# Optimization experiments

Hardware: AMD Instinct MI355X
Metric: run time of the kernel (lower is better)

Reference implementation:

```python
import jax, jax.numpy as jnp
import numpy as np

B, T, C, HD = 4, 4096, 2048, 128  # batch, block_size, n_embadding, head_dim


def _precompute_cos_sin(dim, end, theta=10000.0):
    freqs = 1.0 / theta ** (np.arange(0, dim, 2)[: dim // 2].astype(np.float32) / dim)
    t = np.arange(end, dtype=np.float32)
    ang = np.outer(t, freqs)  # [T, HD/2]
    return jnp.asarray(np.cos(ang), jnp.float32), jnp.asarray(np.sin(ang), jnp.float32)


def setup_inputs() -> dict:
    key = jax.random.key(0)
    k0, k1, k2, k3 = jax.random.split(key, 4)
    scale = 1.0 / np.sqrt(C).astype(np.float32)
    x = jax.random.normal(k0, (B, T, C), jnp.float32)
    Wq = jax.random.normal(k1, (HD, C), jnp.float32) * scale
    Wk = jax.random.normal(k2, (HD, C), jnp.float32) * scale
    Wv = jax.random.normal(k3, (HD, C), jnp.float32) * scale
    cos, sin = _precompute_cos_sin(HD, T)
    return {"x": x, "Wq": Wq, "Wk": Wk, "Wv": Wv, "cos": cos, "sin": sin}


def _rope(v, cos, sin):
    # v: [B, T, HD]; complex multiply on (even, odd) pairs
    v2 = v.reshape(*v.shape[:-1], -1, 2)  # [B, T, HD/2, 2]
    vr, vi = v2[..., 0], v2[..., 1]
    c = cos[None, :, :]  # [1, T, HD/2]
    s = sin[None, :, :]
    out_r = vr * c - vi * s
    out_i = vr * s + vi * c
    return jnp.stack([out_r, out_i], axis=-1).reshape(v.shape)


def reference(x, Wq, Wk, Wv, cos, sin):
    Bx, Tx, Cx = x.shape
    q = jnp.einsum('btc,dc->btd', x, Wq)
    k = jnp.einsum('btc,dc->btd', x, Wk)
    q = _rope(q, cos, sin)
    k = _rope(k, cos, sin)
    # NOTE: original scales by full embedding dim C, not head_dim
    scores = jnp.einsum('btd,bsd->bts', q, k) * (Cx ** -0.5)
    causal = jnp.tril(jnp.ones((Tx, Tx), bool))
    scores = jnp.where(causal[None, :, :], scores, -jnp.inf)
    w = jax.nn.softmax(scores, axis=-1)
    v = jnp.einsum('btc,dc->btd', x, Wv)
    return jnp.einsum('bts,bsd->btd', w, v)
```

## Files before the change

kernel.cpp:

```cpp
#include <hip/hip_runtime.h>

#define B_ 4
#define T_ 4096
#define C_ 2048
#define HD_ 128
#define M_ (B_*T_)

typedef __bf16 bf8 __attribute__((ext_vector_type(8)));
typedef __bf16 bf16x2 __attribute__((ext_vector_type(2)));
typedef __bf16 bf16x4 __attribute__((ext_vector_type(4)));
typedef unsigned short u16x8 __attribute__((ext_vector_type(8)));
typedef unsigned short u16x4 __attribute__((ext_vector_type(4)));
typedef float f32x4 __attribute__((ext_vector_type(4)));

typedef __attribute__((address_space(3))) unsigned char lds_u8_t;
typedef __attribute__((address_space(1))) const unsigned char gm_u8_t;

__device__ __forceinline__ void glds16(const void* g, void* l) {
    __builtin_amdgcn_global_load_lds((gm_u8_t*)g, (lds_u8_t*)l, 16, 0, 0);
}

__device__ __forceinline__ bf8 cvt_bf8(float4 a, float4 b) {
    bf8 t;
    t[0]=(__bf16)a.x; t[1]=(__bf16)a.y; t[2]=(__bf16)a.z; t[3]=(__bf16)a.w;
    t[4]=(__bf16)b.x; t[5]=(__bf16)b.y; t[6]=(__bf16)b.z; t[7]=(__bf16)b.w;
    return t;
}
__device__ __forceinline__ unsigned pk2(float a, float b) {
    bf16x2 t; t[0] = (__bf16)a; t[1] = (__bf16)b;
    return __builtin_bit_cast(unsigned, t);
}
__device__ __forceinline__ u16x4 pk4(float a, float b, float c, float d) {
    bf16x4 t; t[0]=(__bf16)a; t[1]=(__bf16)b; t[2]=(__bf16)c; t[3]=(__bf16)d;
    return __builtin_bit_cast(u16x4, t);
}
__device__ __forceinline__ bf8 ld_bf8(const unsigned short* p) {
    u16x8 t = *(const u16x8*)p;
    return __builtin_bit_cast(bf8, t);
}
__device__ __forceinline__ float bf2f(unsigned short h) {
    unsigned u = ((unsigned)h) << 16;
    return __builtin_bit_cast(float, u);
}
__device__ __forceinline__ f32x4 zero4() { f32x4 v = {0.f,0.f,0.f,0.f}; return v; }

__global__ __launch_bounds__(256) void wconv(
    const float* __restrict__ Wq, const float* __restrict__ Wk,
    const float* __restrict__ Wv, unsigned short* __restrict__ wbf)
{
    int idx = blockIdx.x * 256 + threadIdx.x;
    int e = idx * 8;
    int z = e >> 18;
    int r = e & 262143;
    const float* src = (z == 0 ? Wq : z == 1 ? Wk : Wv) + r;
    float4 a = *(const float4*)src;
    float4 b = *(const float4*)(src + 4);
    bf8 o = cvt_bf8(a, b);
    *(u16x8*)(wbf + e) = __builtin_bit_cast(u16x8, o);
}

__global__ __launch_bounds__(256) void qkv_gemm(
    const float* __restrict__ x, const unsigned short* __restrict__ wbf,
    const float* __restrict__ cosp, const float* __restrict__ sinp,
    unsigned short* __restrict__ qws, unsigned short* __restrict__ kws,
    unsigned short* __restrict__ vws)
{
    __shared__ __align__(16) float xs[2][64*64];
    __shared__ __align__(16) unsigned short ws2[2][128*64];

    const int tid = threadIdx.x;
    const int w = tid >> 6, l = tid & 63;
    const int g = blockIdx.x;
    const int xcd = g & 7;
    const int s = g >> 3;
    const int z = s % 3;
    const int mm = s / 3;
    const int mt = mm * 8 + xcd;
    const int rowbase = mt * 64;

    const int swz = l & 7;
    const int aq  = l >> 4;
    const int coll = l & 15;

    f32x4 acc[2][4];
    #pragma unroll
    for (int i = 0; i < 2; ++i)
        #pragma unroll
        for (int j = 0; j < 4; ++j) acc[i][j] = zero4();

    const unsigned short* wsrc = wbf + (size_t)z * (HD_ * C_);

    auto stage = [&](int buf, int kc) {
        #pragma unroll
        for (int c = 0; c < 4; ++c) {
            int row = w * 16 + c * 4 + aq;
            int fb = coll ^ (row & 7);
            glds16(x + (size_t)(rowbase + row) * C_ + kc + fb * 4,
                   (void*)&xs[buf][(w * 16 + c * 4) * 64]);
        }
        #pragma unroll
        for (int c = 0; c < 4; ++c) {
            int row = w * 32 + c * 8 + (l >> 3);
            int fb = (l & 7) ^ (row & 7);
            glds16(wsrc + (size_t)row * C_ + kc + fb * 8,
                   (void*)&ws2[buf][(w * 32 + c * 8) * 64]);
        }
    };

    stage(0, 0);

    for (int it = 0; it < 32; ++it) {
        __syncthreads();
        if (it + 1 < 32) stage((it + 1) & 1, (it + 1) * 64);
        const float* xcur = xs[it & 1];
        const unsigned short* wcur = ws2[it & 1];

        #pragma unroll
        for (int ks_ = 0; ks_ < 2; ++ks_) {
            bf8 a[2];
            #pragma unroll
            for (int mi = 0; mi < 2; ++mi) {
                int row = (w & 1) * 32 + mi * 16 + coll;
                int s0 = ks_ * 8 + aq * 2;
                float4 fa = *(const float4*)&xcur[row * 64 + ((s0 ^ swz) << 2)];
                float4 fb = *(const float4*)&xcur[row * 64 + (((s0 + 1) ^ swz) << 2)];
                a[mi] = cvt_bf8(fa, fb);
            }
            #pragma unroll
            for (int nt = 0; nt < 4; ++nt) {
                int row = (w >> 1) * 64 + nt * 16 + coll;
                int slot = (ks_ * 4 + aq) ^ swz;
                bf8 bb = ld_bf8(&wcur[row * 64 + (slot << 3)]);
                acc[0][nt] = __builtin_amdgcn_mfma_f32_16x16x32_bf16(a[0], bb, acc[0][nt], 0, 0, 0);
                acc[1][nt] = __builtin_amdgcn_mfma_f32_16x16x32_bf16(a[1], bb, acc[1][nt], 0, 0, 0);
            }
        }
    }

    const int rl0 = aq * 4;
    const int cbase = (w >> 1) * 64;
    const int mrow = (w & 1) * 32;
    if (z < 2) {
        const float QSC = 0.022097086912079608f * 1.44269504088896340736f;
        const float fs = (z == 0) ? QSC : 1.0f;
        unsigned short* dst = (z == 0) ? qws : kws;
        #pragma unroll
        for (int mi = 0; mi < 2; ++mi) {
            #pragma unroll
            for (int nt = 0; nt < 4; ++nt) {
                int col = cbase + nt * 16 + coll;
                #pragma unroll
                for (int r = 0; r < 4; ++r) {
                    float val = acc[mi][nt][r];
                    float oth = __shfl_xor(val, 1, 64);
                    int grow = rowbase + mrow + mi * 16 + rl0 + r;
                    int t = grow & (T_ - 1);
                    if ((coll & 1) == 0) {
                        int i = col >> 1;
                        float cv = cosp[t * 64 + i], sv = sinp[t * 64 + i];
                        float o_r = (val * cv - oth * sv) * fs;
                        float o_i = (val * sv + oth * cv) * fs;
                        *(unsigned*)&dst[(size_t)grow * HD_ + col] = pk2(o_r, o_i);
                    }
                }
            }
        }
    } else {
        const int bq = rowbase >> 12;
        #pragma unroll
        for (int mi = 0; mi < 2; ++mi) {
            int tb = (rowbase + mrow + mi * 16 + rl0) & (T_ - 1);
            #pragma unroll
            for (int nt = 0; nt < 4; ++nt) {
                int col = cbase + nt * 16 + coll;
                u16x4 pk = pk4(acc[mi][nt][0], acc[mi][nt][1], acc[mi][nt][2], acc[mi][nt][3]);
                *(u16x4*)&vws[(size_t)(bq * HD_ + col) * T_ + tb] = pk;
            }
        }
    }
}

__global__ __launch_bounds__(256) void attn_part(
    const unsigned short* __restrict__ qws, const unsigned short* __restrict__ kws,
    const unsigned short* __restrict__ vws,
    unsigned short* __restrict__ partO, float* __restrict__ partL)
{
    __shared__ __align__(16) unsigned short ks[2][64*128];
    __shared__ __align__(16) unsigned short vs[2][128*64];
    __shared__ __align__(16) unsigned short ps[4*16*72];

    const int tid = threadIdx.x;
    const int w = tid >> 6, l = tid & 63;
    const int id = blockIdx.x;
    const int xcd = id & 7;
    const int b = xcd >> 1;
    const int j = (id >> 3) * 2 + (xcd & 1);
    const int sp = 287 - j;
    int g = 0;
    while (4 * (g + 1) * (g + 2) <= sp) ++g;
    const int r_ = sp - 4 * g * (g + 1);
    const int qdiv = r_ / (g + 1);
    const int qt = 8 * g + qdiv;
    const int c  = r_ - qdiv * (g + 1);
    const int ntiles = (c < g) ? 8 : ((qt & 7) + 1);
    const int slot = b * 288 + 4 * g * (g + 1) + (qt & 7) * (g + 1) + c;
    const int qbase = qt * 64;
    const int cbase = c * 512;
    const size_t rowoff = (size_t)b * T_;

    const int swz = l & 7, aq = l >> 4, coll = l & 15;
    unsigned short* psw = ps + w * (16 * 72);

    bf8 qf[4];
    {
        const unsigned short* qp = qws + (rowoff + qbase + w * 16 + coll) * HD_ + aq * 8;
        #pragma unroll
        for (int kk = 0; kk < 4; ++kk) qf[kk] = ld_bf8(qp + kk * 32);
    }

    auto stageKV = [&](int buf, int st) {
        const int sbase = cbase + st * 64;
        #pragma unroll
        for (int cc = 0; cc < 4; ++cc) {
            int row = w * 16 + cc * 4 + aq;
            int fb = coll ^ (row & 7);
            glds16(kws + (rowoff + sbase + row) * HD_ + fb * 8,
                   (void*)&ks[buf][(w * 16 + cc * 4) * 128]);
        }
        #pragma unroll
        for (int cc = 0; cc < 4; ++cc) {
            int row = w * 32 + cc * 8 + (l >> 3);
            int fb = (l & 7) ^ (row & 7);
            glds16(vws + ((size_t)(b * HD_ + row)) * T_ + sbase + fb * 8,
                   (void*)&vs[buf][(w * 32 + cc * 8) * 64]);
        }
    };
    stageKV(0, 0);

    float l_r[4] = {0.f, 0.f, 0.f, 0.f};
    f32x4 accO[8];
    #pragma unroll
    for (int i = 0; i < 8; ++i) accO[i] = zero4();

    for (int st = 0; st < ntiles; ++st) {
        __syncthreads();
        if (st + 1 < ntiles) stageKV((st + 1) & 1, st + 1);
        const unsigned short* kcur = ks[st & 1];
        const unsigned short* vcur = vs[st & 1];
        const int sbase = cbase + st * 64;
        const bool masked = (sbase == qbase);

        f32x4 sacc[4];
        #pragma unroll
        for (int i = 0; i < 4; ++i) sacc[i] = zero4();
        #pragma unroll
        for (int kk = 0; kk < 4; ++kk) {
            const int slot8 = ((kk * 4 + aq) ^ swz) << 3;
            #pragma unroll
            for (int nt = 0; nt < 4; ++nt) {
                bf8 bb = ld_bf8(&kcur[(nt * 16 + coll) * 128 + slot8]);
                sacc[nt] = __builtin_amdgcn_mfma_f32_16x16x32_bf16(qf[kk], bb, sacc[nt], 0, 0, 0);
            }
        }

        #pragma unroll
        for (int r = 0; r < 4; ++r) {
            float s0 = sacc[0][r], s1 = sacc[1][r], s2 = sacc[2][r], s3 = sacc[3][r];
            if (masked) {
                int qi = qbase + w * 16 + aq * 4 + r;
                int ki = sbase + coll;
                s0 = (ki      > qi) ? -1e30f : s0;
                s1 = (ki + 16 > qi) ? -1e30f : s1;
                s2 = (ki + 32 > qi) ? -1e30f : s2;
                s3 = (ki + 48 > qi) ? -1e30f : s3;
            }
            float p0 = __builtin_amdgcn_exp2f(s0);
            float p1 = __builtin_amdgcn_exp2f(s1);
            float p2 = __builtin_amdgcn_exp2f(s2);
            float p3 = __builtin_amdgcn_exp2f(s3);
            __bf16 c0 = (__bf16)p0, c1 = (__bf16)p1, c2 = (__bf16)p2, c3 = (__bf16)p3;
            const int prow = (aq * 4 + r) * 72;
            psw[prow + coll]      = __builtin_bit_cast(unsigned short, c0);
            psw[prow + 16 + coll] = __builtin_bit_cast(unsigned short, c1);
            psw[prow + 32 + coll] = __builtin_bit_cast(unsigned short, c2);
            psw[prow + 48 + coll] = __builtin_bit_cast(unsigned short, c3);
            l_r[r] += ((float)c0 + (float)c1) + ((float)c2 + (float)c3);
        }

        #pragma unroll
        for (int kk = 0; kk < 2; ++kk) {
            bf8 a = ld_bf8(&psw[coll * 72 + kk * 32 + aq * 8]);
            const int slot8 = ((kk * 4 + aq) ^ swz) << 3;
            #pragma unroll
            for (int nt = 0; nt < 8; ++nt) {
                bf8 bb = ld_bf8(&vcur[(nt * 16 + coll) * 64 + slot8]);
                accO[nt] = __builtin_amdgcn_mfma_f32_16x16x32_bf16(a, bb, accO[nt], 0, 0, 0);
            }
        }
    }

    unsigned short* op = partO + (size_t)slot * (64 * 128);
    #pragma unroll
    for (int r = 0; r < 4; ++r) {
        float s = l_r[r];
        s += __shfl_xor(s, 1, 64);
        s += __shfl_xor(s, 2, 64);
        s += __shfl_xor(s, 4, 64);
        s += __shfl_xor(s, 8, 64);
        int row = w * 16 + aq * 4 + r;
        #pragma unroll
        for (int nt = 0; nt < 8; ++nt) {
            __bf16 ob = (__bf16)accO[nt][r];
            op[row * 128 + nt * 16 + coll] = __builtin_bit_cast(unsigned short, ob);
        }
        if (coll == 0) partL[slot * 64 + row] = s;
    }
}

__global__ __launch_bounds__(256) void attn_merge(
    const unsigned short* __restrict__ partO, const float* __restrict__ partL,
    float* __restrict__ out)
{
    const int bq = blockIdx.x;
    const int b = bq >> 6, qt = bq & 63;
    const int g = qt >> 3;
    const int nc = g + 1;
    const int slotbase = b * 288 + 4 * g * (g + 1) + (qt & 7) * (g + 1);
    const int row = threadIdx.x >> 2;
    const int cg = (threadIdx.x & 3) * 32;

    float acc[32];
    #pragma unroll
    for (int e = 0; e < 32; ++e) acc[e] = 0.f;
    float L = 0.f;
    for (int c = 0; c < nc; ++c) {
        const int slot = slotbase + c;
        L += partL[slot * 64 + row];
        const unsigned short* op = partO + (size_t)slot * (64 * 128) + row * 128 + cg;
        #pragma unroll
        for (int k = 0; k < 4; ++k) {
            u16x8 t = *(const u16x8*)(op + k * 8);
            #pragma unroll
            for (int e = 0; e < 8; ++e) acc[k * 8 + e] += bf2f(t[e]);
        }
    }
    float inv = 1.f / L;
    float* dst = out + ((size_t)(b * T_ + qt * 64 + row)) * HD_ + cg;
    #pragma unroll
    for (int k = 0; k < 8; ++k) {
        float4 o;
        o.x = acc[k * 4 + 0] * inv; o.y = acc[k * 4 + 1] * inv;
        o.z = acc[k * 4 + 2] * inv; o.w = acc[k * 4 + 3] * inv;
        *(float4*)(dst + k * 4) = o;
    }
}

extern "C" void kernel_launch(void* const* d_in, const int* in_sizes, int n_in,
                              void* d_out, int out_size, void* d_ws, size_t ws_size,
                              hipStream_t stream) {
    const float* x    = (const float*)d_in[0];
    const float* Wq   = (const float*)d_in[1];
    const float* Wk   = (const float*)d_in[2];
    const float* Wv   = (const float*)d_in[3];
    const float* cosp = (const float*)d_in[4];
    const float* sinp = (const float*)d_in[5];
    float* out = (float*)d_out;

    unsigned short* qws = (unsigned short*)d_ws;
    unsigned short* kws = qws + (size_t)M_ * HD_;
    unsigned short* vws = kws + (size_t)M_ * HD_;
    unsigned short* wbf = vws + (size_t)M_ * HD_;
    unsigned short* partO = wbf + (size_t)3 * HD_ * C_;
    float* partL = (float*)(partO + (size_t)1152 * 64 * 128);

    wconv<<<dim3(384), dim3(256), 0, stream>>>(Wq, Wk, Wv, wbf);
    qkv_gemm<<<dim3(768), dim3(256), 0, stream>>>(x, wbf, cosp, sinp, qws, kws, vws);
    attn_part<<<dim3(1152), dim3(256), 0, stream>>>(qws, kws, vws, partO, partL);
    attn_merge<<<dim3(256), dim3(256), 0, stream>>>(partO, partL, out);
}
```

Baseline: 327.4 us.

## Replace double-buffered LDS staging with single-buffer load-sync-compute loops

Both the QKV projection GEMM and the attention partial kernel drop their ping-pong LDS buffers. Each iteration now issues the tile load, synchronizes, then computes. This halves shared memory per block, which may allow more resident blocks per CU. In exchange, load latency is no longer overlapped with MFMA work inside a block, and an extra barrier is added per iteration.

```diff
diff --git a/kernel.cpp b/kernel.cpp
--- a/kernel.cpp
+++ b/kernel.cpp
@@ -65,8 +65,8 @@
     unsigned short* __restrict__ qws, unsigned short* __restrict__ kws,
     unsigned short* __restrict__ vws)
 {
-    __shared__ __align__(16) float xs[2][64*64];
-    __shared__ __align__(16) unsigned short ws2[2][128*64];
+    __shared__ __align__(16) float xs[64*64];
+    __shared__ __align__(16) unsigned short ws2[128*64];
 
     const int tid = threadIdx.x;
     const int w = tid >> 6, l = tid & 63;
@@ -90,30 +90,23 @@
 
     const unsigned short* wsrc = wbf + (size_t)z * (HD_ * C_);
 
-    auto stage = [&](int buf, int kc) {
+    for (int kc = 0; kc < C_; kc += 64) {
+        __syncthreads();
         #pragma unroll
         for (int c = 0; c < 4; ++c) {
             int row = w * 16 + c * 4 + aq;
             int fb = coll ^ (row & 7);
             glds16(x + (size_t)(rowbase + row) * C_ + kc + fb * 4,
-                   (void*)&xs[buf][(w * 16 + c * 4) * 64]);
+                   (void*)&xs[(w * 16 + c * 4) * 64]);
         }
         #pragma unroll
         for (int c = 0; c < 4; ++c) {
             int row = w * 32 + c * 8 + (l >> 3);
             int fb = (l & 7) ^ (row & 7);
             glds16(wsrc + (size_t)row * C_ + kc + fb * 8,
-                   (void*)&ws2[buf][(w * 32 + c * 8) * 64]);
-        }
-    };
-
-    stage(0, 0);
-
-    for (int it = 0; it < 32; ++it) {
+                   (void*)&ws2[(w * 32 + c * 8) * 64]);
+        }
         __syncthreads();
-        if (it + 1 < 32) stage((it + 1) & 1, (it + 1) * 64);
-        const float* xcur = xs[it & 1];
-        const unsigned short* wcur = ws2[it & 1];
 
         #pragma unroll
         for (int ks_ = 0; ks_ < 2; ++ks_) {
@@ -122,15 +115,15 @@
             for (int mi = 0; mi < 2; ++mi) {
                 int row = (w & 1) * 32 + mi * 16 + coll;
                 int s0 = ks_ * 8 + aq * 2;
-                float4 fa = *(const float4*)&xcur[row * 64 + ((s0 ^ swz) << 2)];
-                float4 fb = *(const float4*)&xcur[row * 64 + (((s0 + 1) ^ swz) << 2)];
+                float4 fa = *(const float4*)&xs[row * 64 + ((s0 ^ swz) << 2)];
+                float4 fb = *(const float4*)&xs[row * 64 + (((s0 + 1) ^ swz) << 2)];
                 a[mi] = cvt_bf8(fa, fb);
             }
             #pragma unroll
             for (int nt = 0; nt < 4; ++nt) {
                 int row = (w >> 1) * 64 + nt * 16 + coll;
                 int slot = (ks_ * 4 + aq) ^ swz;
-                bf8 bb = ld_bf8(&wcur[row * 64 + (slot << 3)]);
+                bf8 bb = ld_bf8(&ws2[row * 64 + (slot << 3)]);
                 acc[0][nt] = __builtin_amdgcn_mfma_f32_16x16x32_bf16(a[0], bb, acc[0][nt], 0, 0, 0);
                 acc[1][nt] = __builtin_amdgcn_mfma_f32_16x16x32_bf16(a[1], bb, acc[1][nt], 0, 0, 0);
             }
@@ -185,8 +178,8 @@
     const unsigned short* __restrict__ vws,
     unsigned short* __restrict__ partO, float* __restrict__ partL)
 {
-    __shared__ __align__(16) unsigned short ks[2][64*128];
-    __shared__ __align__(16) unsigned short vs[2][128*64];
+    __shared__ __align__(16) unsigned short ks[64*128];
+    __shared__ __align__(16) unsigned short vs[128*64];
     __shared__ __align__(16) unsigned short ps[4*16*72];
 
     const int tid = threadIdx.x;
@@ -218,36 +211,30 @@
         for (int kk = 0; kk < 4; ++kk) qf[kk] = ld_bf8(qp + kk * 32);
     }
 
-    auto stageKV = [&](int buf, int st) {
+    float l_r[4] = {0.f, 0.f, 0.f, 0.f};
+    f32x4 accO[8];
+    #pragma unroll
+    for (int i = 0; i < 8; ++i) accO[i] = zero4();
+
+    for (int st = 0; st < ntiles; ++st) {
         const int sbase = cbase + st * 64;
+        __syncthreads();
         #pragma unroll
         for (int cc = 0; cc < 4; ++cc) {
             int row = w * 16 + cc * 4 + aq;
             int fb = coll ^ (row & 7);
             glds16(kws + (rowoff + sbase + row) * HD_ + fb * 8,
-                   (void*)&ks[buf][(w * 16 + cc * 4) * 128]);
+                   (void*)&ks[(w * 16 + cc * 4) * 128]);
         }
         #pragma unroll
         for (int cc = 0; cc < 4; ++cc) {
             int row = w * 32 + cc * 8 + (l >> 3);
             int fb = (l & 7) ^ (row & 7);
             glds16(vws + ((size_t)(b * HD_ + row)) * T_ + sbase + fb * 8,
-                   (void*)&vs[buf][(w * 32 + cc * 8) * 64]);
-        }
-    };
-    stageKV(0, 0);
-
-    float l_r[4] = {0.f, 0.f, 0.f, 0.f};
-    f32x4 accO[8];
-    #pragma unroll
-    for (int i = 0; i < 8; ++i) accO[i] = zero4();
-
-    for (int st = 0; st < ntiles; ++st) {
+                   (void*)&vs[(w * 32 + cc * 8) * 64]);
+        }
         __syncthreads();
-        if (st + 1 < ntiles) stageKV((st + 1) & 1, st + 1);
-        const unsigned short* kcur = ks[st & 1];
-        const unsigned short* vcur = vs[st & 1];
-        const int sbase = cbase + st * 64;
+
         const bool masked = (sbase == qbase);
 
         f32x4 sacc[4];
@@ -258,7 +245,7 @@
             const int slot8 = ((kk * 4 + aq) ^ swz) << 3;
             #pragma unroll
             for (int nt = 0; nt < 4; ++nt) {
-                bf8 bb = ld_bf8(&kcur[(nt * 16 + coll) * 128 + slot8]);
+                bf8 bb = ld_bf8(&ks[(nt * 16 + coll) * 128 + slot8]);
                 sacc[nt] = __builtin_amdgcn_mfma_f32_16x16x32_bf16(qf[kk], bb, sacc[nt], 0, 0, 0);
             }
         }
@@ -293,7 +280,7 @@
             const int slot8 = ((kk * 4 + aq) ^ swz) << 3;
             #pragma unroll
             for (int nt = 0; nt < 8; ++nt) {
-                bf8 bb = ld_bf8(&vcur[(nt * 16 + coll) * 64 + slot8]);
+                bf8 bb = ld_bf8(&vs[(nt * 16 + coll) * 64 + slot8]);
                 accO[nt] = __builtin_amdgcn_mfma_f32_16x16x32_bf16(a, bb, accO[nt], 0, 0, 0);
             }
         }
```

Measured after the change: 281.7 us. -14.0%, faster.
